# Kernel optimization log

Measured on AMD Instinct MI355X. Metric: run time of the kernel, lower is better.

Reference implementation:

```python
import jax, jax.numpy as jnp
import numpy as np

N_NODES = 200   # nlim = 50*4
EMB = 5
N_APPTYPES = 3
FEAT_IN = 50 * 52 + N_NODES  # 2800
B = 16384
E = 800


def setup_inputs() -> dict:
    key = jax.random.key(0)
    ks = jax.random.split(key, 16)
    x = jax.random.normal(ks[0], (B, 50, 52), dtype=jnp.float32)
    apps = jax.random.randint(ks[1], (B, N_NODES), 0, N_APPTYPES)
    edge_src = jax.random.randint(ks[2], (E,), 0, N_NODES)
    edge_dst = jax.random.randint(ks[3], (E,), 0, N_NODES)
    def lin(k, fan_in, fan_out):
        bound = 1.0 / np.sqrt(fan_in)
        kw, kb = jax.random.split(k)
        W = jax.random.uniform(kw, (fan_in, fan_out), minval=-bound, maxval=bound, dtype=jnp.float32)
        b = jax.random.uniform(kb, (fan_out,), minval=-bound, maxval=bound, dtype=jnp.float32)
        return W, b
    emb_table = jax.random.normal(ks[4], (N_APPTYPES, EMB), dtype=jnp.float32)
    gc_w, gc_b = lin(ks[5], EMB, 1)
    W1, b1 = lin(ks[6], FEAT_IN, 128)
    W2, b2 = lin(ks[7], 128, 128)
    W3, b3 = lin(ks[8], 128, 64)
    W4, b4 = lin(ks[9], 64, 2)
    return {"x": x, "apps": apps, "edge_src": edge_src, "edge_dst": edge_dst,
            "emb_table": emb_table, "gc_w": gc_w, "gc_b": gc_b,
            "W1": W1, "b1": b1, "W2": W2, "b2": b2,
            "W3": W3, "b3": b3, "W4": W4, "b4": b4}


def _graph_conv(h, edge_src, edge_dst, gc_w, gc_b):
    # DGL GraphConv, norm='both': D_in^{-1/2} A D_out^{-1/2} (X W) + b
    ones = jnp.ones((edge_src.shape[0],), dtype=h.dtype)
    deg_out = jnp.clip(jax.ops.segment_sum(ones, edge_src, num_segments=N_NODES), 1.0)
    deg_in = jnp.clip(jax.ops.segment_sum(ones, edge_dst, num_segments=N_NODES), 1.0)
    norm_src = deg_out ** -0.5  # [N]
    norm_dst = deg_in ** -0.5
    hw = h @ gc_w                       # [B, N, 1] (weight applied first: 5 > 1)
    msg = (hw * norm_src[None, :, None])[:, edge_src, :]      # [B, E, 1]
    agg = jnp.zeros_like(hw).at[:, edge_dst, :].add(msg)      # scatter-add over dst
    return agg * norm_dst[None, :, None] + gc_b


def reference(x, apps, edge_src, edge_dst, emb_table, gc_w, gc_b,
              W1, b1, W2, b2, W3, b3, W4, b4):
    h = emb_table[apps]                 # [B, 200, 5]; apps already length nlim -> zero-pad is no-op
    g = _graph_conv(h, edge_src, edge_dst, gc_w, gc_b)        # [B, 200, 1]
    feat = jnp.concatenate([x.reshape(x.shape[0], -1), g.reshape(g.shape[0], -1)], axis=-1)  # [B, 2800]
    a = jax.nn.softplus(feat @ W1 + b1)
    a = jax.nn.softplus(a @ W2 + b2)
    a = a @ W3 + b3
    a = a - jnp.tanh(a)                 # Tanhshrink
    out = jax.nn.sigmoid(a @ W4 + b4)   # [B, 2]
    return out
```

## Files before the change

### kernel.cpp

```cpp
#include <hip/hip_runtime.h>

#define NNODES 200
#define FEATX  2600
#define FEAT   2800
#define NCH    44
#define N1     128

typedef _Float16 f16;
typedef _Float16 f16x8 __attribute__((ext_vector_type(8)));
typedef float    f32x4 __attribute__((ext_vector_type(4)));

#define W1T_OFF   0u
#define W2T_OFF   720896u
#define W3T_OFF   753664u
#define WG_OFF    770048u
#define B1P_OFF   872448u
#define HW_OFF    872960u
#define WE_OFF    874816u

__device__ __forceinline__ void gl_lds16(const void* g, void* l) {
  __builtin_amdgcn_global_load_lds(
      (const __attribute__((address_space(1))) unsigned int*)g,
      (__attribute__((address_space(3))) unsigned int*)l, 16, 0, 0);
}

__global__ void prep1(const int* __restrict__ esrc, const int* __restrict__ edst,
                      const float* __restrict__ emb, const float* __restrict__ gcw,
                      const float* __restrict__ gcb, const float* __restrict__ W1,
                      const float* __restrict__ b1, char* __restrict__ ws) {
  __shared__ float dg[2][NNODES];
  const int tid = threadIdx.x;
  for (int i = tid; i < 2 * NNODES; i += 256) ((float*)dg)[i] = 0.f;
  __syncthreads();
  for (int e = tid; e < 800; e += 256) {
    atomicAdd(&dg[0][esrc[e]], 1.f);
    atomicAdd(&dg[1][edst[e]], 1.f);
  }
  __syncthreads();
  for (int i = tid; i < 2 * NNODES; i += 256) {
    float* p = (float*)dg + i;
    *p = 1.f / sqrtf(fmaxf(*p, 1.f));
  }
  if (tid < 3) {
    float s = 0.f;
    for (int q = 0; q < 5; ++q) s += emb[tid * 5 + q] * gcw[q];
    ((float*)(ws + HW_OFF))[tid] = s;
  }
  __syncthreads();
  float* we = (float*)(ws + WE_OFF);
  for (int e = tid; e < 800; e += 256)
    we[e] = dg[0][esrc[e]] * dg[1][edst[e]];
  if (tid < 128) {
    float s = 0.f;
    for (int d = 0; d < NNODES; ++d) s += W1[(FEATX + d) * N1 + tid];
    ((float*)(ws + B1P_OFF))[tid] = b1[tid] + gcb[0] * s;
  }
}

__global__ void prepWg(const int* __restrict__ esrc, const int* __restrict__ edst,
                       const float* __restrict__ W1, char* __restrict__ ws) {
  __shared__ int   se[800];
  __shared__ short sd[800];
  __shared__ float swe[800];
  const int n = blockIdx.x;
  const int j = threadIdx.x;
  const float* we = (const float*)(ws + WE_OFF);
  for (int e = j; e < 800; e += 128) {
    se[e] = esrc[e]; sd[e] = (short)edst[e]; swe[e] = we[e];
  }
  __syncthreads();
  float acc = 0.f;
  for (int e = 0; e < 800; ++e) {
    if (se[e] == n) acc += swe[e] * W1[(FEATX + (int)sd[e]) * N1 + j];
  }
  ((float*)(ws + WG_OFF))[n * N1 + j] = acc;
}

__global__ void pack(const float* __restrict__ W1, const float* __restrict__ W2,
                     const float* __restrict__ W3, char* __restrict__ ws) {
  __shared__ __align__(16) char tile[32768];
  const int bid = blockIdx.x, tid = threadIdx.x;
  if (bid < NCH) {
    const float* wg = (const float*)(ws + WG_OFF);
    const int c = tid & 127, kh = tid >> 7;
    for (int kk = kh; kk < 64; kk += 2) {
      const int k = bid * 64 + kk;
      float v;
      if (k < FEATX) v = W1[k * N1 + c];
      else if (k < FEAT) v = wg[(k - FEATX) * N1 + c];
      else v = 0.f;
      *(f16*)(tile + ((c * 128 + kk * 2) ^ ((c & 7) << 4))) = (f16)v;
    }
    __syncthreads();
    char* dst = ws + W1T_OFF + bid * 16384;
    for (int i = 0; i < 4; ++i)
      *(uint4*)(dst + tid * 16 + i * 4096) = *(const uint4*)(tile + tid * 16 + i * 4096);
  } else if (bid == NCH) {
    const int c = tid & 127, kh = tid >> 7;
    for (int k = kh; k < 128; k += 2) {
      const float v = W2[k * 128 + c];
      *(f16*)(tile + ((c * 256 + k * 2) ^ ((c & 7) << 4))) = (f16)v;
    }
    __syncthreads();
    char* dst = ws + W2T_OFF;
    for (int i = 0; i < 8; ++i)
      *(uint4*)(dst + tid * 16 + i * 4096) = *(const uint4*)(tile + tid * 16 + i * 4096);
  } else {
    const int c = tid & 63, kh = tid >> 6;
    for (int k = kh; k < 128; k += 4) {
      const float v = W3[k * 64 + c];
      *(f16*)(tile + ((c * 256 + k * 2) ^ ((c & 7) << 4))) = (f16)v;
    }
    __syncthreads();
    char* dst = ws + W3T_OFF;
    for (int i = 0; i < 4; ++i)
      *(uint4*)(dst + tid * 16 + i * 4096) = *(const uint4*)(tile + tid * 16 + i * 4096);
  }
}

__global__ __launch_bounds__(512, 2)
void fused_main(const float* __restrict__ x, const int* __restrict__ apps,
                const char* __restrict__ ws, const float* __restrict__ b2,
                const float* __restrict__ b3, const float* __restrict__ W4,
                const float* __restrict__ b4, float* __restrict__ out) {
  __shared__ __align__(16) char lds[81920];
  char*  sB    = lds;
  char*  sAct1 = lds + 49152;
  char*  sAct2 = lds + 65536;
  float* sAct3 = (float*)(lds + 49152);

  const int tid  = threadIdx.x;
  const int lane = tid & 63;
  const int w    = tid >> 6;
  const int lrow = lane & 15;
  const int lk   = lane >> 4;
  const int wr   = w >> 1;
  const int wc   = w & 1;
  const int blk  = blockIdx.x;

  const float* hwv = (const float*)(ws + HW_OFF);
  const float hw0 = hwv[0], hw1 = hwv[1], hw2 = hwv[2];

  const int row_g = blk * 64 + wr * 16 + lrow;
  const float* xrow = x + (size_t)row_g * FEATX;
  const int*   irow = apps + (size_t)row_g * NNODES;

  int boff[2][4];
#pragma unroll
  for (int ks = 0; ks < 2; ++ks)
#pragma unroll
    for (int f = 0; f < 4; ++f) {
      const int c = wc * 64 + f * 16 + lrow;
      boff[ks][f] = ((c * 128 + ks * 64 + lk * 16) ^ ((lrow & 7) << 4));
    }

  const f32x4 zed = {0.f, 0.f, 0.f, 0.f};
  f32x4 acc1[4] = {zed, zed, zed, zed};

  auto issueB = [&](int tc, int buf) {
    const char* src = ws + W1T_OFF + (size_t)tc * 16384;
    char* dst = sB + buf * 16384;
#pragma unroll
    for (int r = 0; r < 2; ++r) {
      const int o = r * 8192 + w * 1024;
      gl_lds16(src + o + lane * 16, dst + o);
    }
  };
  auto issueA = [&](int tc, uint4 (&ar)[2][2]) {
#pragma unroll
    for (int ks = 0; ks < 2; ++ks) {
      const int k0 = tc * 64 + ks * 32 + lk * 8;
      const char* p;
      if (k0 + 8 <= FEATX)  p = (const char*)(xrow + k0);
      else if (k0 < FEAT)   p = (const char*)(irow + (k0 - FEATX));
      else                  p = (const char*)xrow;
      ar[ks][0] = *(const uint4*)p;
      ar[ks][1] = *(const uint4*)(p + 16);
    }
  };
  auto cvtA = [&](int t, const uint4 (&ar)[2][2], f16x8 (&af)[2]) {
#pragma unroll
    for (int ks = 0; ks < 2; ++ks) {
      const int k0 = t * 64 + ks * 32 + lk * 8;
      union { uint4 u[2]; unsigned ui[8]; float f[8]; } d;
      d.u[0] = ar[ks][0]; d.u[1] = ar[ks][1];
      union { f16x8 v; f16 h[8]; } r;
      if (k0 + 8 <= FEATX) {
#pragma unroll
        for (int j2 = 0; j2 < 8; ++j2) r.h[j2] = (f16)d.f[j2];
      } else if (k0 < FEAT) {
#pragma unroll
        for (int j2 = 0; j2 < 8; ++j2) {
          const unsigned a = d.ui[j2];
          r.h[j2] = (f16)(a == 0u ? hw0 : (a == 1u ? hw1 : hw2));
        }
      } else {
#pragma unroll
        for (int j2 = 0; j2 < 8; ++j2) r.h[j2] = (f16)0.f;
      }
      af[ks] = r.v;
    }
  };
  auto compute = [&](const f16x8 (&af)[2], int buf) {
    const char* b = sB + buf * 16384;
#pragma unroll
    for (int ks = 0; ks < 2; ++ks)
#pragma unroll
      for (int f = 0; f < 4; ++f) {
        const f16x8 bf = *(const f16x8*)(b + boff[ks][f]);
        acc1[f] = __builtin_amdgcn_mfma_f32_16x16x32_f16(af[ks], bf, acc1[f], 0, 0, 0);
      }
  };

  uint4 arA[2][2], arB[2][2];
  f16x8 af[2];

  issueB(0, 0); issueA(0, arA);
  issueB(1, 1); issueA(1, arB);

  for (int t = 0; t < NCH; t += 2) {
    {
      asm volatile("s_waitcnt vmcnt(6)" ::: "memory");
      __builtin_amdgcn_s_barrier();
      __builtin_amdgcn_sched_barrier(0);
      const int tc = (t + 2 < NCH) ? t + 2 : NCH - 1;
      issueB(tc, (t + 2) % 3);
      cvtA(t, arA, af);
      issueA(tc, arA);
      compute(af, t % 3);
    }
    {
      asm volatile("s_waitcnt vmcnt(6)" ::: "memory");
      __builtin_amdgcn_s_barrier();
      __builtin_amdgcn_sched_barrier(0);
      const int t1 = t + 1;
      const int tc = (t1 + 2 < NCH) ? t1 + 2 : NCH - 1;
      issueB(tc, (t1 + 2) % 3);
      cvtA(t1, arB, af);
      issueA(tc, arB);
      compute(af, t1 % 3);
    }
  }
  __syncthreads();

#pragma unroll
  for (int r = 0; r < 6; ++r) {
    const int o = r * 8192 + w * 1024;
    gl_lds16(ws + W2T_OFF + o + lane * 16, lds + o);
  }

  const float* b1p = (const float*)(ws + B1P_OFF);
#pragma unroll
  for (int f = 0; f < 4; ++f) {
    const int col = wc * 64 + f * 16 + lrow;
    const float bb = b1p[col];
#pragma unroll
    for (int r = 0; r < 4; ++r) {
      const int row = wr * 16 + lk * 4 + r;
      float v = acc1[f][r] + bb;
      v = fmaxf(v, 0.f) + log1pf(expf(-fabsf(v)));
      *(f16*)(sAct1 + ((row * 256 + col * 2) ^ ((row & 7) << 4))) = (f16)v;
    }
  }
  __syncthreads();

  f32x4 acc2[4] = {zed, zed, zed, zed};
#pragma unroll
  for (int ks = 0; ks < 4; ++ks) {
    const int ar = wr * 16 + lrow;
    const f16x8 a2 = *(const f16x8*)(sAct1 + ((ar * 256 + ks * 64 + lk * 16) ^ ((lrow & 7) << 4)));
#pragma unroll
    for (int f = 0; f < 4; ++f) {
      const int c = wc * 64 + f * 16 + lrow;
      const f16x8 bf = *(const f16x8*)(lds + ((c * 256 + ks * 64 + lk * 16) ^ ((lrow & 7) << 4)));
      acc2[f] = __builtin_amdgcn_mfma_f32_16x16x32_f16(a2, bf, acc2[f], 0, 0, 0);
    }
  }
#pragma unroll
  for (int f = 0; f < 4; ++f) {
    const int col = wc * 64 + f * 16 + lrow;
    const float bb = b2[col];
#pragma unroll
    for (int r = 0; r < 4; ++r) {
      const int row = wr * 16 + lk * 4 + r;
      float v = acc2[f][r] + bb;
      v = fmaxf(v, 0.f) + log1pf(expf(-fabsf(v)));
      *(f16*)(sAct2 + ((row * 256 + col * 2) ^ ((row & 7) << 4))) = (f16)v;
    }
  }
  __syncthreads();

  f32x4 acc3[2] = {zed, zed};
  const char* w3p = lds + 32768;
#pragma unroll
  for (int ks = 0; ks < 4; ++ks) {
    const int ar = wr * 16 + lrow;
    const f16x8 a3 = *(const f16x8*)(sAct2 + ((ar * 256 + ks * 64 + lk * 16) ^ ((lrow & 7) << 4)));
#pragma unroll
    for (int f = 0; f < 2; ++f) {
      const int c = wc * 32 + f * 16 + lrow;
      const f16x8 bf = *(const f16x8*)(w3p + ((c * 256 + ks * 64 + lk * 16) ^ ((lrow & 7) << 4)));
      acc3[f] = __builtin_amdgcn_mfma_f32_16x16x32_f16(a3, bf, acc3[f], 0, 0, 0);
    }
  }
#pragma unroll
  for (int f = 0; f < 2; ++f) {
    const int col = wc * 32 + f * 16 + lrow;
    const float bb = b3[col];
#pragma unroll
    for (int r = 0; r < 4; ++r) {
      const int row = wr * 16 + lk * 4 + r;
      const float z = acc3[f][r] + bb;
      sAct3[row * 64 + col] = z - tanhf(z);
    }
  }
  __syncthreads();

  if (tid < 128) {
    const int row = tid >> 1, j = tid & 1;
    float a4 = b4[j];
#pragma unroll 8
    for (int k = 0; k < 64; ++k)
      a4 += sAct3[row * 64 + k] * W4[k * 2 + j];
    out[(size_t)(blk * 64 + row) * 2 + j] = 1.f / (1.f + expf(-a4));
  }
}

extern "C" void kernel_launch(void* const* d_in, const int* in_sizes, int n_in,
                              void* d_out, int out_size, void* d_ws, size_t ws_size,
                              hipStream_t stream) {
  const float* x    = (const float*)d_in[0];
  const int*   apps = (const int*)d_in[1];
  const int*   esrc = (const int*)d_in[2];
  const int*   edst = (const int*)d_in[3];
  const float* emb  = (const float*)d_in[4];
  const float* gcw  = (const float*)d_in[5];
  const float* gcb  = (const float*)d_in[6];
  const float* W1   = (const float*)d_in[7];
  const float* b1   = (const float*)d_in[8];
  const float* W2   = (const float*)d_in[9];
  const float* b2   = (const float*)d_in[10];
  const float* W3   = (const float*)d_in[11];
  const float* b3   = (const float*)d_in[12];
  const float* W4   = (const float*)d_in[13];
  const float* b4   = (const float*)d_in[14];
  char* ws = (char*)d_ws;
  float* out = (float*)d_out;

  hipLaunchKernelGGL(prep1, dim3(1), dim3(256), 0, stream,
                     esrc, edst, emb, gcw, gcb, W1, b1, ws);
  hipLaunchKernelGGL(prepWg, dim3(200), dim3(128), 0, stream, esrc, edst, W1, ws);
  hipLaunchKernelGGL(pack, dim3(46), dim3(256), 0, stream, W1, W2, W3, ws);
  hipLaunchKernelGGL(fused_main, dim3(256), dim3(512), 0, stream,
                     x, apps, ws, b2, b3, W4, b4, out);
}
```

Baseline: 391.4 us.

## Rewrite main kernel as single-wave blocks reading MFMA-packed weights from global

```diff
diff --git a/kernel.cpp b/kernel.cpp
--- a/kernel.cpp
+++ b/kernel.cpp
@@ -3,326 +3,364 @@
 #define NNODES 200
 #define FEATX  2600
 #define FEAT   2800
-#define NCH    44
+#define NC     88
 #define N1     128
 
 typedef _Float16 f16;
 typedef _Float16 f16x8 __attribute__((ext_vector_type(8)));
 typedef float    f32x4 __attribute__((ext_vector_type(4)));
 
-#define W1T_OFF   0u
-#define W2T_OFF   720896u
-#define W3T_OFF   753664u
+#define W1P_OFF   0u
+#define W2P_OFF   720896u
+#define W3P_OFF   753664u
 #define WG_OFF    770048u
-#define B1P_OFF   872448u
-#define HW_OFF    872960u
-#define WE_OFF    874816u
-
-__device__ __forceinline__ void gl_lds16(const void* g, void* l) {
-  __builtin_amdgcn_global_load_lds(
-      (const __attribute__((address_space(1))) unsigned int*)g,
-      (__attribute__((address_space(3))) unsigned int*)l, 16, 0, 0);
-}
-
-__global__ void prep1(const int* __restrict__ esrc, const int* __restrict__ edst,
-                      const float* __restrict__ emb, const float* __restrict__ gcw,
-                      const float* __restrict__ gcb, const float* __restrict__ W1,
-                      const float* __restrict__ b1, char* __restrict__ ws) {
-  __shared__ float dg[2][NNODES];
+#define B1P_OFF   821248u
+#define HW_OFF    821760u
+#define CSRP_OFF  821792u
+#define CSRD_OFF  822608u
+#define CSRW_OFF  825808u
+
+__global__ __launch_bounds__(256)
+void prepA(const int* __restrict__ esrc, const int* __restrict__ edst,
+           const float* __restrict__ emb, const float* __restrict__ gcw,
+           const float* __restrict__ gcb, const float* __restrict__ W1,
+           const float* __restrict__ b1, char* __restrict__ ws) {
+  __shared__ float dgo[NNODES], dgi[NNODES];
+  __shared__ int   ssrc[800], sdst[800];
+  __shared__ int   cnt[NNODES], cur[NNODES];
+  __shared__ int   ps[256];
+  __shared__ float red[256];
   const int tid = threadIdx.x;
-  for (int i = tid; i < 2 * NNODES; i += 256) ((float*)dg)[i] = 0.f;
+
+  if (tid < NNODES) { dgo[tid] = 0.f; dgi[tid] = 0.f; cnt[tid] = 0; cur[tid] = 0; }
   __syncthreads();
   for (int e = tid; e < 800; e += 256) {
-    atomicAdd(&dg[0][esrc[e]], 1.f);
-    atomicAdd(&dg[1][edst[e]], 1.f);
+    const int s = esrc[e], d = edst[e];
+    ssrc[e] = s; sdst[e] = d;
+    atomicAdd(&dgo[s], 1.f);
+    atomicAdd(&dgi[d], 1.f);
+    atomicAdd(&cnt[s], 1);
   }
   __syncthreads();
-  for (int i = tid; i < 2 * NNODES; i += 256) {
-    float* p = (float*)dg + i;
-    *p = 1.f / sqrtf(fmaxf(*p, 1.f));
+  if (tid < NNODES) {
+    dgo[tid] = 1.f / sqrtf(fmaxf(dgo[tid], 1.f));
+    dgi[tid] = 1.f / sqrtf(fmaxf(dgi[tid], 1.f));
   }
   if (tid < 3) {
     float s = 0.f;
     for (int q = 0; q < 5; ++q) s += emb[tid * 5 + q] * gcw[q];
     ((float*)(ws + HW_OFF))[tid] = s;
   }
+  ps[tid] = (tid < NNODES) ? cnt[tid] : 0;
   __syncthreads();
-  float* we = (float*)(ws + WE_OFF);
-  for (int e = tid; e < 800; e += 256)
-    we[e] = dg[0][esrc[e]] * dg[1][edst[e]];
-  if (tid < 128) {
+  for (int off = 1; off < 256; off <<= 1) {
+    const int v = (tid >= off) ? ps[tid - off] : 0;
+    __syncthreads();
+    ps[tid] += v;
+    __syncthreads();
+  }
+  int* rp = (int*)(ws + CSRP_OFF);
+  if (tid < NNODES) rp[tid] = ps[tid] - cnt[tid];
+  if (tid == NNODES) rp[NNODES] = 800;
+  __syncthreads();
+  int*   cd = (int*)(ws + CSRD_OFF);
+  float* cw = (float*)(ws + CSRW_OFF);
+  for (int e = tid; e < 800; e += 256) {
+    const int s = ssrc[e], d = sdst[e];
+    const int pos = (ps[s] - cnt[s]) + atomicAdd(&cur[s], 1);
+    cd[pos] = d;
+    cw[pos] = dgo[s] * dgi[d];
+  }
+  {
+    const int j = tid & 127, h = tid >> 7;
     float s = 0.f;
-    for (int d = 0; d < NNODES; ++d) s += W1[(FEATX + d) * N1 + tid];
-    ((float*)(ws + B1P_OFF))[tid] = b1[tid] + gcb[0] * s;
-  }
-}
-
-__global__ void prepWg(const int* __restrict__ esrc, const int* __restrict__ edst,
-                       const float* __restrict__ W1, char* __restrict__ ws) {
-  __shared__ int   se[800];
-  __shared__ short sd[800];
-  __shared__ float swe[800];
+    for (int d = h; d < NNODES; d += 2)
+      s += W1[(FEATX + d) * N1 + j];
+    red[tid] = s;
+    __syncthreads();
+    if (h == 0)
+      ((float*)(ws + B1P_OFF))[j] = b1[j] + gcb[0] * (red[j] + red[128 + j]);
+  }
+}
+
+__global__ __launch_bounds__(128)
+void prepWg(const float* __restrict__ W1, char* __restrict__ ws) {
   const int n = blockIdx.x;
   const int j = threadIdx.x;
-  const float* we = (const float*)(ws + WE_OFF);
-  for (int e = j; e < 800; e += 128) {
-    se[e] = esrc[e]; sd[e] = (short)edst[e]; swe[e] = we[e];
-  }
-  __syncthreads();
+  const int* rp   = (const int*)(ws + CSRP_OFF);
+  const int* cd   = (const int*)(ws + CSRD_OFF);
+  const float* cw = (const float*)(ws + CSRW_OFF);
+  const int e0 = rp[n], e1 = rp[n + 1];
   float acc = 0.f;
-  for (int e = 0; e < 800; ++e) {
-    if (se[e] == n) acc += swe[e] * W1[(FEATX + (int)sd[e]) * N1 + j];
-  }
-  ((float*)(ws + WG_OFF))[n * N1 + j] = acc;
-}
-
-__global__ void pack(const float* __restrict__ W1, const float* __restrict__ W2,
-                     const float* __restrict__ W3, char* __restrict__ ws) {
-  __shared__ __align__(16) char tile[32768];
+  for (int e = e0; e < e1; ++e)
+    acc += cw[e] * W1[(FEATX + cd[e]) * N1 + j];
+  ((f16*)(ws + WG_OFF))[n * N1 + j] = (f16)acc;
+}
+
+__global__ __launch_bounds__(256)
+void pack(const float* __restrict__ W1, const float* __restrict__ W2,
+          const float* __restrict__ W3, char* __restrict__ ws) {
+  __shared__ __align__(16) float T[32 * 128];
   const int bid = blockIdx.x, tid = threadIdx.x;
-  if (bid < NCH) {
-    const float* wg = (const float*)(ws + WG_OFF);
-    const int c = tid & 127, kh = tid >> 7;
-    for (int kk = kh; kk < 64; kk += 2) {
-      const int k = bid * 64 + kk;
-      float v;
-      if (k < FEATX) v = W1[k * N1 + c];
-      else if (k < FEAT) v = wg[(k - FEATX) * N1 + c];
-      else v = 0.f;
-      *(f16*)(tile + ((c * 128 + kk * 2) ^ ((c & 7) << 4))) = (f16)v;
-    }
-    __syncthreads();
-    char* dst = ws + W1T_OFF + bid * 16384;
-    for (int i = 0; i < 4; ++i)
-      *(uint4*)(dst + tid * 16 + i * 4096) = *(const uint4*)(tile + tid * 16 + i * 4096);
-  } else if (bid == NCH) {
-    const int c = tid & 127, kh = tid >> 7;
-    for (int k = kh; k < 128; k += 2) {
-      const float v = W2[k * 128 + c];
-      *(f16*)(tile + ((c * 256 + k * 2) ^ ((c & 7) << 4))) = (f16)v;
-    }
-    __syncthreads();
-    char* dst = ws + W2T_OFF;
-    for (int i = 0; i < 8; ++i)
-      *(uint4*)(dst + tid * 16 + i * 4096) = *(const uint4*)(tile + tid * 16 + i * 4096);
+  const f16* wg = (const f16*)(ws + WG_OFF);
+  if (bid < NC) {
+    const int k0 = bid * 32;
+#pragma unroll
+    for (int i = 0; i < 4; ++i) {
+      const int p = i * 1024 + tid * 4;
+      const int r = p >> 7, c = p & 127;
+      const int k = k0 + r;
+      float4 v;
+      if (k < FEATX) v = *(const float4*)(W1 + (size_t)k * N1 + c);
+      else if (k < FEAT) {
+        const f16* g = wg + (k - FEATX) * N1 + c;
+        v.x = (float)g[0]; v.y = (float)g[1]; v.z = (float)g[2]; v.w = (float)g[3];
+      } else { v.x = v.y = v.z = v.w = 0.f; }
+      *(float4*)(&T[r * 128 + c]) = v;
+    }
+    __syncthreads();
+    char* dst = ws + W1P_OFF + (size_t)bid * 8192;
+    for (int s = tid; s < 512; s += 256) {
+      const int f = s >> 6, lx = s & 63;
+      const int colb = f * 16 + (lx & 15), kb = (lx >> 4) * 8;
+      union { f16x8 v; f16 h[8]; } u;
+#pragma unroll
+      for (int j = 0; j < 8; ++j) u.h[j] = (f16)T[(kb + j) * 128 + colb];
+      *(f16x8*)(dst + f * 1024 + lx * 16) = u.v;
+    }
+  } else if (bid < 92) {
+    const int cc = bid - 88, k0 = cc * 32;
+#pragma unroll
+    for (int i = 0; i < 4; ++i) {
+      const int p = i * 1024 + tid * 4;
+      const int r = p >> 7, c = p & 127;
+      *(float4*)(&T[r * 128 + c]) = *(const float4*)(W2 + (size_t)(k0 + r) * 128 + c);
+    }
+    __syncthreads();
+    char* dst = ws + W2P_OFF + (size_t)cc * 8192;
+    for (int s = tid; s < 512; s += 256) {
+      const int f = s >> 6, lx = s & 63;
+      const int colb = f * 16 + (lx & 15), kb = (lx >> 4) * 8;
+      union { f16x8 v; f16 h[8]; } u;
+#pragma unroll
+      for (int j = 0; j < 8; ++j) u.h[j] = (f16)T[(kb + j) * 128 + colb];
+      *(f16x8*)(dst + f * 1024 + lx * 16) = u.v;
+    }
   } else {
-    const int c = tid & 63, kh = tid >> 6;
-    for (int k = kh; k < 128; k += 4) {
-      const float v = W3[k * 64 + c];
-      *(f16*)(tile + ((c * 256 + k * 2) ^ ((c & 7) << 4))) = (f16)v;
-    }
-    __syncthreads();
-    char* dst = ws + W3T_OFF;
-    for (int i = 0; i < 4; ++i)
-      *(uint4*)(dst + tid * 16 + i * 4096) = *(const uint4*)(tile + tid * 16 + i * 4096);
-  }
-}
-
-__global__ __launch_bounds__(512, 2)
+    const int cc = bid - 92, k0 = cc * 32;
+#pragma unroll
+    for (int i = 0; i < 2; ++i) {
+      const int p = i * 1024 + tid * 4;
+      const int r = p >> 6, c = p & 63;
+      *(float4*)(&T[r * 64 + c]) = *(const float4*)(W3 + (size_t)(k0 + r) * 64 + c);
+    }
+    __syncthreads();
+    char* dst = ws + W3P_OFF + (size_t)cc * 4096;
+    {
+      const int s = tid;
+      const int f = s >> 6, lx = s & 63;
+      const int colb = f * 16 + (lx & 15), kb = (lx >> 4) * 8;
+      union { f16x8 v; f16 h[8]; } u;
+#pragma unroll
+      for (int j = 0; j < 8; ++j) u.h[j] = (f16)T[(kb + j) * 64 + colb];
+      *(f16x8*)(dst + f * 1024 + lx * 16) = u.v;
+    }
+  }
+}
+
+__global__ __launch_bounds__(64)
 void fused_main(const float* __restrict__ x, const int* __restrict__ apps,
                 const char* __restrict__ ws, const float* __restrict__ b2,
                 const float* __restrict__ b3, const float* __restrict__ W4,
                 const float* __restrict__ b4, float* __restrict__ out) {
-  __shared__ __align__(16) char lds[81920];
-  char*  sB    = lds;
-  char*  sAct1 = lds + 49152;
-  char*  sAct2 = lds + 65536;
-  float* sAct3 = (float*)(lds + 49152);
-
-  const int tid  = threadIdx.x;
-  const int lane = tid & 63;
-  const int w    = tid >> 6;
-  const int lrow = lane & 15;
-  const int lk   = lane >> 4;
-  const int wr   = w >> 1;
-  const int wc   = w & 1;
-  const int blk  = blockIdx.x;
+  __shared__ __align__(16) char lds[8192];
+  const int l   = threadIdx.x;
+  const int blk = blockIdx.x;
+  const int lm  = l & 15, lg = l >> 4;
+  const int row0 = blk * 32;
 
   const float* hwv = (const float*)(ws + HW_OFF);
   const float hw0 = hwv[0], hw1 = hwv[1], hw2 = hwv[2];
 
-  const int row_g = blk * 64 + wr * 16 + lrow;
-  const float* xrow = x + (size_t)row_g * FEATX;
-  const int*   irow = apps + (size_t)row_g * NNODES;
-
-  int boff[2][4];
-#pragma unroll
-  for (int ks = 0; ks < 2; ++ks)
-#pragma unroll
-    for (int f = 0; f < 4; ++f) {
-      const int c = wc * 64 + f * 16 + lrow;
-      boff[ks][f] = ((c * 128 + ks * 64 + lk * 16) ^ ((lrow & 7) << 4));
-    }
+  const float* xr0 = x + (size_t)(row0 + lm) * FEATX;
+  const float* xr1 = x + (size_t)(row0 + 16 + lm) * FEATX;
+  const int*   ir0 = apps + (size_t)(row0 + lm) * NNODES;
+  const int*   ir1 = apps + (size_t)(row0 + 16 + lm) * NNODES;
+  const char*  w1p = ws + W1P_OFF;
 
   const f32x4 zed = {0.f, 0.f, 0.f, 0.f};
-  f32x4 acc1[4] = {zed, zed, zed, zed};
-
-  auto issueB = [&](int tc, int buf) {
-    const char* src = ws + W1T_OFF + (size_t)tc * 16384;
-    char* dst = sB + buf * 16384;
-#pragma unroll
-    for (int r = 0; r < 2; ++r) {
-      const int o = r * 8192 + w * 1024;
-      gl_lds16(src + o + lane * 16, dst + o);
-    }
+  f32x4 acc[2][8];
+#pragma unroll
+  for (int rt = 0; rt < 2; ++rt)
+#pragma unroll
+    for (int f = 0; f < 8; ++f) acc[rt][f] = zed;
+
+  f16x8 B0[8], B1[8];
+  uint4 A0[4], A1[4];
+  f16x8 af[2];
+
+  auto LB = [&](int c, f16x8* B) {
+    const char* p = w1p + (size_t)(c > NC - 1 ? NC - 1 : c) * 8192 + l * 16;
+#pragma unroll
+    for (int f = 0; f < 8; ++f) B[f] = *(const f16x8*)(p + f * 1024);
   };
-  auto issueA = [&](int tc, uint4 (&ar)[2][2]) {
-#pragma unroll
-    for (int ks = 0; ks < 2; ++ks) {
-      const int k0 = tc * 64 + ks * 32 + lk * 8;
-      const char* p;
-      if (k0 + 8 <= FEATX)  p = (const char*)(xrow + k0);
-      else if (k0 < FEAT)   p = (const char*)(irow + (k0 - FEATX));
-      else                  p = (const char*)xrow;
-      ar[ks][0] = *(const uint4*)p;
-      ar[ks][1] = *(const uint4*)(p + 16);
-    }
+  auto LA = [&](int c, uint4* A) {
+    const int k0 = (c > NC - 1 ? NC - 1 : c) * 32 + lg * 8;
+    const char *p0, *p1;
+    if (k0 + 8 <= FEATX) { p0 = (const char*)(xr0 + k0); p1 = (const char*)(xr1 + k0); }
+    else if (k0 < FEAT)  { p0 = (const char*)(ir0 + (k0 - FEATX)); p1 = (const char*)(ir1 + (k0 - FEATX)); }
+    else                 { p0 = (const char*)xr0; p1 = (const char*)xr1; }
+    A[0] = *(const uint4*)p0; A[1] = *(const uint4*)(p0 + 16);
+    A[2] = *(const uint4*)p1; A[3] = *(const uint4*)(p1 + 16);
   };
-  auto cvtA = [&](int t, const uint4 (&ar)[2][2], f16x8 (&af)[2]) {
-#pragma unroll
-    for (int ks = 0; ks < 2; ++ks) {
-      const int k0 = t * 64 + ks * 32 + lk * 8;
+  auto CV = [&](int c, const uint4* A, f16x8* a2) {
+    const int k0 = c * 32 + lg * 8;
+#pragma unroll
+    for (int rt = 0; rt < 2; ++rt) {
       union { uint4 u[2]; unsigned ui[8]; float f[8]; } d;
-      d.u[0] = ar[ks][0]; d.u[1] = ar[ks][1];
+      d.u[0] = A[rt * 2]; d.u[1] = A[rt * 2 + 1];
       union { f16x8 v; f16 h[8]; } r;
       if (k0 + 8 <= FEATX) {
 #pragma unroll
-        for (int j2 = 0; j2 < 8; ++j2) r.h[j2] = (f16)d.f[j2];
+        for (int j = 0; j < 8; ++j) r.h[j] = (f16)d.f[j];
       } else if (k0 < FEAT) {
 #pragma unroll
-        for (int j2 = 0; j2 < 8; ++j2) {
-          const unsigned a = d.ui[j2];
-          r.h[j2] = (f16)(a == 0u ? hw0 : (a == 1u ? hw1 : hw2));
+        for (int j = 0; j < 8; ++j) {
+          const unsigned a = d.ui[j];
+          r.h[j] = (f16)(a == 0u ? hw0 : (a == 1u ? hw1 : hw2));
         }
       } else {
 #pragma unroll
-        for (int j2 = 0; j2 < 8; ++j2) r.h[j2] = (f16)0.f;
+        for (int j = 0; j < 8; ++j) r.h[j] = (f16)0.f;
       }
-      af[ks] = r.v;
+      a2[rt] = r.v;
     }
   };
-  auto compute = [&](const f16x8 (&af)[2], int buf) {
-    const char* b = sB + buf * 16384;
-#pragma unroll
-    for (int ks = 0; ks < 2; ++ks)
-#pragma unroll
-      for (int f = 0; f < 4; ++f) {
-        const f16x8 bf = *(const f16x8*)(b + boff[ks][f]);
-        acc1[f] = __builtin_amdgcn_mfma_f32_16x16x32_f16(af[ks], bf, acc1[f], 0, 0, 0);
+  auto MM = [&](const f16x8* a2, const f16x8* B) {
+#pragma unroll
+    for (int f = 0; f < 8; ++f) {
+      acc[0][f] = __builtin_amdgcn_mfma_f32_16x16x32_f16(a2[0], B[f], acc[0][f], 0, 0, 0);
+      acc[1][f] = __builtin_amdgcn_mfma_f32_16x16x32_f16(a2[1], B[f], acc[1][f], 0, 0, 0);
+    }
+  };
+
+  LA(0, A0); LB(0, B0); LA(1, A1);
+#pragma unroll 1
+  for (int c = 0; c < NC; c += 2) {
+    LB(c + 1, B1);
+    CV(c, A0, af);
+    LA(c + 2, A0);
+    MM(af, B0);
+    LB(c + 2, B0);
+    CV(c + 1, A1, af);
+    LA(c + 3, A1);
+    MM(af, B1);
+  }
+
+  const float* b1p = (const float*)(ws + B1P_OFF);
+#pragma unroll
+  for (int f = 0; f < 8; ++f) {
+    const int col = f * 16 + lm;
+    const float bb = b1p[col];
+#pragma unroll
+    for (int rt = 0; rt < 2; ++rt)
+#pragma unroll
+      for (int r = 0; r < 4; ++r) {
+        const int row = rt * 16 + lg * 4 + r;
+        float v = acc[rt][f][r] + bb;
+        v = fmaxf(v, 0.f) + log1pf(expf(-fabsf(v)));
+        *(f16*)(lds + ((row * 256 + col * 2) ^ ((row & 7) << 4))) = (f16)v;
       }
-  };
-
-  uint4 arA[2][2], arB[2][2];
-  f16x8 af[2];
-
-  issueB(0, 0); issueA(0, arA);
-  issueB(1, 1); issueA(1, arB);
-
-  for (int t = 0; t < NCH; t += 2) {
-    {
-      asm volatile("s_waitcnt vmcnt(6)" ::: "memory");
-      __builtin_amdgcn_s_barrier();
-      __builtin_amdgcn_sched_barrier(0);
-      const int tc = (t + 2 < NCH) ? t + 2 : NCH - 1;
-      issueB(tc, (t + 2) % 3);
-      cvtA(t, arA, af);
-      issueA(tc, arA);
-      compute(af, t % 3);
-    }
-    {
-      asm volatile("s_waitcnt vmcnt(6)" ::: "memory");
-      __builtin_amdgcn_s_barrier();
-      __builtin_amdgcn_sched_barrier(0);
-      const int t1 = t + 1;
-      const int tc = (t1 + 2 < NCH) ? t1 + 2 : NCH - 1;
-      issueB(tc, (t1 + 2) % 3);
-      cvtA(t1, arB, af);
-      issueA(tc, arB);
-      compute(af, t1 % 3);
-    }
-  }
-  __syncthreads();
-
-#pragma unroll
-  for (int r = 0; r < 6; ++r) {
-    const int o = r * 8192 + w * 1024;
-    gl_lds16(ws + W2T_OFF + o + lane * 16, lds + o);
-  }
-
-  const float* b1p = (const float*)(ws + B1P_OFF);
+  }
+
+  f32x4 c2[2][8];
+#pragma unroll
+  for (int rt = 0; rt < 2; ++rt)
+#pragma unroll
+    for (int f = 0; f < 8; ++f) c2[rt][f] = zed;
+  const char* w2p = ws + W2P_OFF;
+#pragma unroll
+  for (int ks = 0; ks < 4; ++ks) {
+    f16x8 bb2[8];
+#pragma unroll
+    for (int f = 0; f < 8; ++f)
+      bb2[f] = *(const f16x8*)(w2p + ks * 8192 + f * 1024 + l * 16);
+    f16x8 a2[2];
+#pragma unroll
+    for (int rt = 0; rt < 2; ++rt) {
+      const int row = rt * 16 + lm;
+      a2[rt] = *(const f16x8*)(lds + ((row * 256 + ks * 64 + lg * 16) ^ ((row & 7) << 4)));
+    }
+#pragma unroll
+    for (int f = 0; f < 8; ++f) {
+      c2[0][f] = __builtin_amdgcn_mfma_f32_16x16x32_f16(a2[0], bb2[f], c2[0][f], 0, 0, 0);
+      c2[1][f] = __builtin_amdgcn_mfma_f32_16x16x32_f16(a2[1], bb2[f], c2[1][f], 0, 0, 0);
+    }
+  }
+#pragma unroll
+  for (int f = 0; f < 8; ++f) {
+    const int col = f * 16 + lm;
+    const float bb = b2[col];
+#pragma unroll
+    for (int rt = 0; rt < 2; ++rt)
+#pragma unroll
+      for (int r = 0; r < 4; ++r) {
+        const int row = rt * 16 + lg * 4 + r;
+        float v = c2[rt][f][r] + bb;
+        v = fmaxf(v, 0.f) + log1pf(expf(-fabsf(v)));
+        *(f16*)(lds + ((row * 256 + col * 2) ^ ((row & 7) << 4))) = (f16)v;
+      }
+  }
+
+  f32x4 c3[2][4];
+#pragma unroll
+  for (int rt = 0; rt < 2; ++rt)
+#pragma unroll
+    for (int f = 0; f < 4; ++f) c3[rt][f] = zed;
+  const char* w3p = ws + W3P_OFF;
+#pragma unroll
+  for (int ks = 0; ks < 4; ++ks) {
+    f16x8 bb3[4];
+#pragma unroll
+    for (int f = 0; f < 4; ++f)
+      bb3[f] = *(const f16x8*)(w3p + ks * 4096 + f * 1024 + l * 16);
+    f16x8 a3[2];
+#pragma unroll
+    for (int rt = 0; rt < 2; ++rt) {
+      const int row = rt * 16 + lm;
+      a3[rt] = *(const f16x8*)(lds + ((row * 256 + ks * 64 + lg * 16) ^ ((row & 7) << 4)));
+    }
+#pragma unroll
+    for (int f = 0; f < 4; ++f) {
+      c3[0][f] = __builtin_amdgcn_mfma_f32_16x16x32_f16(a3[0], bb3[f], c3[0][f], 0, 0, 0);
+      c3[1][f] = __builtin_amdgcn_mfma_f32_16x16x32_f16(a3[1], bb3[f], c3[1][f], 0, 0, 0);
+    }
+  }
 #pragma unroll
   for (int f = 0; f < 4; ++f) {
-    const int col = wc * 64 + f * 16 + lrow;
-    const float bb = b1p[col];
-#pragma unroll
-    for (int r = 0; r < 4; ++r) {
-      const int row = wr * 16 + lk * 4 + r;
-      float v = acc1[f][r] + bb;
-      v = fmaxf(v, 0.f) + log1pf(expf(-fabsf(v)));
-      *(f16*)(sAct1 + ((row * 256 + col * 2) ^ ((row & 7) << 4))) = (f16)v;
-    }
-  }
-  __syncthreads();
-
-  f32x4 acc2[4] = {zed, zed, zed, zed};
-#pragma unroll
-  for (int ks = 0; ks < 4; ++ks) {
-    const int ar = wr * 16 + lrow;
-    const f16x8 a2 = *(const f16x8*)(sAct1 + ((ar * 256 + ks * 64 + lk * 16) ^ ((lrow & 7) << 4)));
-#pragma unroll
-    for (int f = 0; f < 4; ++f) {
-      const int c = wc * 64 + f * 16 + lrow;
-      const f16x8 bf = *(const f16x8*)(lds + ((c * 256 + ks * 64 + lk * 16) ^ ((lrow & 7) << 4)));
-      acc2[f] = __builtin_amdgcn_mfma_f32_16x16x32_f16(a2, bf, acc2[f], 0, 0, 0);
-    }
-  }
-#pragma unroll
-  for (int f = 0; f < 4; ++f) {
-    const int col = wc * 64 + f * 16 + lrow;
-    const float bb = b2[col];
-#pragma unroll
-    for (int r = 0; r < 4; ++r) {
-      const int row = wr * 16 + lk * 4 + r;
-      float v = acc2[f][r] + bb;
-      v = fmaxf(v, 0.f) + log1pf(expf(-fabsf(v)));
-      *(f16*)(sAct2 + ((row * 256 + col * 2) ^ ((row & 7) << 4))) = (f16)v;
-    }
-  }
-  __syncthreads();
-
-  f32x4 acc3[2] = {zed, zed};
-  const char* w3p = lds + 32768;
-#pragma unroll
-  for (int ks = 0; ks < 4; ++ks) {
-    const int ar = wr * 16 + lrow;
-    const f16x8 a3 = *(const f16x8*)(sAct2 + ((ar * 256 + ks * 64 + lk * 16) ^ ((lrow & 7) << 4)));
-#pragma unroll
-    for (int f = 0; f < 2; ++f) {
-      const int c = wc * 32 + f * 16 + lrow;
-      const f16x8 bf = *(const f16x8*)(w3p + ((c * 256 + ks * 64 + lk * 16) ^ ((lrow & 7) << 4)));
-      acc3[f] = __builtin_amdgcn_mfma_f32_16x16x32_f16(a3, bf, acc3[f], 0, 0, 0);
-    }
-  }
-#pragma unroll
-  for (int f = 0; f < 2; ++f) {
-    const int col = wc * 32 + f * 16 + lrow;
+    const int col = f * 16 + lm;
     const float bb = b3[col];
 #pragma unroll
-    for (int r = 0; r < 4; ++r) {
-      const int row = wr * 16 + lk * 4 + r;
-      const float z = acc3[f][r] + bb;
-      sAct3[row * 64 + col] = z - tanhf(z);
-    }
-  }
-  __syncthreads();
-
-  if (tid < 128) {
-    const int row = tid >> 1, j = tid & 1;
-    float a4 = b4[j];
-#pragma unroll 8
-    for (int k = 0; k < 64; ++k)
-      a4 += sAct3[row * 64 + k] * W4[k * 2 + j];
-    out[(size_t)(blk * 64 + row) * 2 + j] = 1.f / (1.f + expf(-a4));
+    for (int rt = 0; rt < 2; ++rt)
+#pragma unroll
+      for (int r = 0; r < 4; ++r) {
+        const int row = rt * 16 + lg * 4 + r;
+        const float z = c3[rt][f][r] + bb;
+        *(float*)(lds + ((row * 256 + col * 4) ^ ((row & 7) << 4))) = z - tanhf(z);
+      }
+  }
+
+  {
+    const int row = l >> 1, j = l & 1;
+    float s = 0.f;
+#pragma unroll
+    for (int kk = 0; kk < 16; ++kk) {
+      const f32x4 a = *(const f32x4*)(lds + ((row * 256 + kk * 16) ^ ((row & 7) << 4)));
+      s += a[0] * W4[(kk * 4 + 0) * 2 + j] + a[1] * W4[(kk * 4 + 1) * 2 + j]
+         + a[2] * W4[(kk * 4 + 2) * 2 + j] + a[3] * W4[(kk * 4 + 3) * 2 + j];
+    }
+    s += b4[j];
+    out[(size_t)(row0 + row) * 2 + j] = 1.f / (1.f + expf(-s));
   }
 }
 
@@ -347,10 +385,10 @@
   char* ws = (char*)d_ws;
   float* out = (float*)d_out;
 
-  hipLaunchKernelGGL(prep1, dim3(1), dim3(256), 0, stream,
+  hipLaunchKernelGGL(prepA, dim3(1), dim3(256), 0, stream,
                      esrc, edst, emb, gcw, gcb, W1, b1, ws);
-  hipLaunchKernelGGL(prepWg, dim3(200), dim3(128), 0, stream, esrc, edst, W1, ws);
-  hipLaunchKernelGGL(pack, dim3(46), dim3(256), 0, stream, W1, W2, W3, ws);
-  hipLaunchKernelGGL(fused_main, dim3(256), dim3(512), 0, stream,
+  hipLaunchKernelGGL(prepWg, dim3(200), dim3(128), 0, stream, W1, ws);
+  hipLaunchKernelGGL(pack, dim3(96), dim3(256), 0, stream, W1, W2, W3, ws);
+  hipLaunchKernelGGL(fused_main, dim3(512), dim3(64), 0, stream,
                      x, apps, ws, b2, b3, W4, b4, out);
 }
```

After: 379.2 us. -3.1%, faster.
